# Kernel tuning notes

Measured on AMD Instinct MI355X. Metric: run time of the kernel, lower is better.

The kernel has to match this reference:

```python
import jax, jax.numpy as jnp
import numpy as np

B, T, D_IN, D_OUT = 4, 2048, 1024, 1024


def setup_inputs() -> dict:
    key = jax.random.key(0)
    k1, k2, k3, k4 = jax.random.split(key, 4)
    s = 0.02  # keep activations in a sane range
    x = jax.random.normal(k1, (B, T, D_IN), dtype=jnp.float32)
    Wq = jax.random.normal(k2, (D_IN, D_OUT), dtype=jnp.float32) * s
    Wk = jax.random.normal(k3, (D_IN, D_OUT), dtype=jnp.float32) * s
    Wv = jax.random.normal(k4, (D_IN, D_OUT), dtype=jnp.float32) * s
    return {"x": x, "Wq": Wq, "Wk": Wk, "Wv": Wv}


def reference(x, Wq, Wk, Wv):
    # Linear projections (torch Linear: y = x @ W^T, here W stored as [d_in, d_out])
    q = jnp.einsum('btd,de->bte', x, Wq)
    k = jnp.einsum('btd,de,->bte', x, Wk, jnp.float32(1.0)) if False else jnp.einsum('btd,de->bte', x, Wk)
    v = jnp.einsum('btd,de->bte', x, Wv)
    # Full [B, T, T] score matrix (faithful to the hand-rolled implementation)
    scores = jnp.einsum('bqe,bke->bqk', q, k)
    T_ = x.shape[1]
    causal = jnp.triu(jnp.ones((T_, T_), dtype=bool), k=1)  # True above diagonal
    scores = jnp.where(causal[None, :, :], -jnp.inf, scores)
    scale = 1.0 / jnp.sqrt(jnp.asarray(k.shape[-1], dtype=scores.dtype))
    attn = jax.nn.softmax(scores * scale, axis=-1)
    # dropout p=0.0 -> identity
    return jnp.einsum('bqk,bke->bqe', attn, v)
```

## Files before the change

kernel.cpp:

```cpp
#include <hip/hip_runtime.h>
#include <hip/hip_bf16.h>
#include <cstdint>

typedef __attribute__((ext_vector_type(8))) short short8;
typedef __attribute__((ext_vector_type(4))) short short4v;
typedef __attribute__((ext_vector_type(4))) float floatx4;
typedef unsigned short ushort;

__device__ __forceinline__ float bf2f(ushort u) {
  unsigned int x = ((unsigned int)u) << 16;
  return __builtin_bit_cast(float, x);
}
__device__ __forceinline__ ushort f2bf(float f) {
  unsigned int x = __builtin_bit_cast(unsigned int, f);
  x += 0x7fffu + ((x >> 16) & 1u);
  return (ushort)(x >> 16);
}

__device__ __forceinline__ void gload_lds16(const void* g, void* l) {
  __builtin_amdgcn_global_load_lds(
      (const __attribute__((address_space(1))) void*)g,
      (__attribute__((address_space(3))) void*)l, 16, 0, 0);
}


__global__ __launch_bounds__(256) void prep_kernel(const float* __restrict__ x,
                                                   const float* __restrict__ Wq,
                                                   const float* __restrict__ Wk,
                                                   const float* __restrict__ Wv,
                                                   ushort* __restrict__ xb,
                                                   ushort* __restrict__ Wt) {
  int bid = blockIdx.x;
  int tid = threadIdx.x;
  if (bid < 4096) {
    int i = bid * 256 + tid;
    const float4* xf = (const float4*)x;
    float4 a = xf[i * 2], b = xf[i * 2 + 1];
    short8 o;
    o[0] = (short)f2bf(a.x); o[1] = (short)f2bf(a.y);
    o[2] = (short)f2bf(a.z); o[3] = (short)f2bf(a.w);
    o[4] = (short)f2bf(b.x); o[5] = (short)f2bf(b.y);
    o[6] = (short)f2bf(b.z); o[7] = (short)f2bf(b.w);
    ((short8*)xb)[i] = o;
  } else {
    int t = bid - 4096;
    int z = t >> 8;
    int rem = t & 255;
    int c0 = (rem & 15) * 64;
    int r0 = (rem >> 4) * 64;
    const float* W = z == 0 ? Wq : (z == 1 ? Wk : Wv);
    ushort* O = Wt + (size_t)z * 1024 * 1024;
    __shared__ float tile[64][65];
#pragma unroll
    for (int i = 0; i < 4; ++i) {
      int c = tid + i * 256; int rr = c >> 4, q = c & 15;
      float4 v = *(const float4*)&W[(size_t)(r0 + rr) * 1024 + c0 + q * 4];
      tile[rr][q * 4 + 0] = v.x; tile[rr][q * 4 + 1] = v.y;
      tile[rr][q * 4 + 2] = v.z; tile[rr][q * 4 + 3] = v.w;
    }
    __syncthreads();
#pragma unroll
    for (int i = 0; i < 2; ++i) {
      int c = tid + i * 256; int oc = c >> 3, q = c & 7;
      short8 o;
#pragma unroll
      for (int j = 0; j < 8; ++j) o[j] = (short)f2bf(tile[q * 8 + j][oc]);
      *(short8*)&O[(size_t)(c0 + oc) * 1024 + r0 + q * 8] = o;
    }
  }
}


__global__ __launch_bounds__(512, 2) void qkv8_kernel(const ushort* __restrict__ A,
                                                      const ushort* __restrict__ Bm,
                                                      ushort* __restrict__ Qo,
                                                      ushort* __restrict__ Ko,
                                                      ushort* __restrict__ Vt) {
  __shared__ __align__(16) ushort lds[2][2][2][8192];

  const int tid = threadIdx.x;
  const int lane = tid & 63;
  const int wave = tid >> 6;
  const int wm = wave >> 2;
  const int wn = wave & 3;
  const int r15 = lane & 15;
  const int kg = lane >> 4;

  const int nwgx = 32, nwgy = 12;
  int orig = blockIdx.y * nwgx + blockIdx.x;
  int swz = (orig & 7) * ((nwgx * nwgy) >> 3) + (orig >> 3);
  int by = swz % nwgy;
  int bx = swz / nwgy;
  const int m0 = bx * 256;
  const int n0 = by * 256;

  const ushort* Ag = A + (size_t)m0 * 1024;
  const ushort* Bg = Bm + (size_t)n0 * 1024;

  const int NKT = 16;

  floatx4 acc[8][4] = {};

  auto stage = [&](int sidx) {
    int kt = sidx >> 2, hh = sidx & 3;
    int mat = hh & 1, kh = hh >> 1;
    ushort* dst = &lds[kt & 1][mat][kh][0];
    const ushort* src = mat ? Bg : Ag;
    int kbase = kt * 64 + kh * 32;
#pragma unroll
    for (int i = 0; i < 2; ++i) {
      int t = tid + i * 512;
      int d = t * 16;
      int L = d ^ (((d >> 7) & 3) << 4);
      int row = L >> 6;
      int colE = (L & 63) >> 1;
      gload_lds16(src + (size_t)row * 1024 + kbase + colE, dst + t * 8);
    }
  };

  auto ldA = [&](int buf, int ks, int m) -> short8 {
    int row = wm * 128 + m * 16 + r15;
    int L = row * 64 + kg * 16;
    int P = L ^ (((row >> 1) & 3) << 4);
    return *(const short8*)((const char*)&lds[buf][0][ks][0] + P);
  };
  auto ldB = [&](int buf, int ks, int n) -> short8 {
    int row = wn * 64 + n * 16 + r15;
    int L = row * 64 + kg * 16;
    int P = L ^ (((row >> 1) & 3) << 4);
    return *(const short8*)((const char*)&lds[buf][1][ks][0] + P);
  };

  for (int s = 0; s < 6; ++s) stage(s);
  asm volatile("s_waitcnt vmcnt(8)" ::: "memory");
  __builtin_amdgcn_s_barrier();

  short8 bfrag[4];
  int sidx = 6;
  for (int kt = 0; kt < NKT; ++kt) {
    int cur = kt & 1;
#pragma unroll
    for (int q = 0; q < 4; ++q) {
      const int ks = q >> 1;
      const int msub = (q & 1) * 4;
      short8 afrag[4];
      if ((q & 1) == 0) {
#pragma unroll
        for (int n = 0; n < 4; ++n) bfrag[n] = ldB(cur, ks, n);
      }
#pragma unroll
      for (int m = 0; m < 4; ++m) afrag[m] = ldA(cur, ks, msub + m);
      if (sidx < NKT * 4) stage(sidx);
      ++sidx;
      if (q & 1) asm volatile("s_waitcnt vmcnt(4)" ::: "memory");
      __builtin_amdgcn_s_barrier();
      __builtin_amdgcn_s_setprio(1);
#pragma unroll
      for (int m = 0; m < 4; ++m)
#pragma unroll
        for (int n = 0; n < 4; ++n)
          acc[msub + m][n] =
              __builtin_amdgcn_mfma_f32_16x16x32_bf16(afrag[m], bfrag[n], acc[msub + m][n], 0, 0, 0);
      __builtin_amdgcn_s_setprio(0);
      __builtin_amdgcn_s_barrier();
    }
  }

  const int z = n0 >> 10;
  const int rq = kg * 4;
  if (z < 2) {
    ushort* Cz = z == 0 ? Qo : Ko;
    const int cb = n0 & 1023;
#pragma unroll
    for (int m = 0; m < 8; ++m) {
#pragma unroll
      for (int n = 0; n < 4; ++n) {
        int gc = cb + wn * 64 + n * 16 + r15;
#pragma unroll
        for (int r = 0; r < 4; ++r) {
          int gr = m0 + wm * 128 + m * 16 + rq + r;
          Cz[(size_t)gr * 1024 + gc] = f2bf(acc[m][n][r]);
        }
      }
    }
  } else {
#pragma unroll
    for (int m = 0; m < 8; ++m) {
      int gr = m0 + wm * 128 + m * 16 + rq;
      int b = gr >> 11;
      int t = gr & 2047;
      ushort* Vb = Vt + (size_t)b * 1024 * 2048;
#pragma unroll
      for (int n = 0; n < 4; ++n) {
        int e = (n0 - 2048) + wn * 64 + n * 16 + r15;
        short4v o;
#pragma unroll
        for (int r = 0; r < 4; ++r) o[r] = (short)f2bf(acc[m][n][r]);
        *(short4v*)&Vb[(size_t)e * 2048 + t] = o;
      }
    }
  }
}


__global__ __launch_bounds__(256) void s_kernel(const ushort* __restrict__ Q,
                                                const ushort* __restrict__ K,
                                                ushort* __restrict__ S,
                                                float* __restrict__ Lpart) {
  int t = blockIdx.x;
  int qb = (int)((sqrtf(8.f * (float)t + 1.f) - 1.f) * 0.5f);
  while ((qb + 1) * (qb + 2) / 2 <= t) ++qb;
  while (qb * (qb + 1) / 2 > t) --qb;
  int kb = t - qb * (qb + 1) / 2;
  const size_t bi = blockIdx.y;
  const ushort* Ag = Q + bi * 2048 * 1024 + (size_t)qb * 128 * 1024;
  const ushort* Bg = K + bi * 2048 * 1024 + (size_t)kb * 128 * 1024;
  ushort* C = S + bi * 2048 * 2048;
  const int m0 = qb * 128, n0 = kb * 128;

  __shared__ __align__(16) ushort Asm[2][128 * 32];
  __shared__ __align__(16) ushort Bsm[2][128 * 32];
  __shared__ float rsum_lds[4][64];
  const int tid = threadIdx.x;
  const int lane = tid & 63;
  const int wave = tid >> 6;
  const int wrow = (wave >> 1) * 64;
  const int wcol = (wave & 1) * 64;
  const int r15 = lane & 15;
  const int kg = (lane >> 4) * 8;

  floatx4 acc[4][4] = {};

  auto stage = [&](int buf, int kt) {
    int k0 = kt * 32;
#pragma unroll
    for (int i = 0; i < 2; ++i) {
      int c = tid + i * 256;
      gload_lds16(Ag + (size_t)(c >> 2) * 1024 + k0 + (c & 3) * 8, &Asm[buf][c * 8]);
    }
#pragma unroll
    for (int i = 0; i < 2; ++i) {
      int c = tid + i * 256;
      gload_lds16(Bg + (size_t)(c >> 2) * 1024 + k0 + (c & 3) * 8, &Bsm[buf][c * 8]);
    }
  };

  stage(0, 0);
  for (int kt = 0; kt < 32; ++kt) {
    int cur = kt & 1;
    __syncthreads();
    if (kt + 1 < 32) stage(cur ^ 1, kt + 1);
    short8 af[4], bfr[4];
#pragma unroll
    for (int m = 0; m < 4; ++m)
      af[m] = *(const short8*)&Asm[cur][(wrow + m * 16 + r15) * 32 + kg];
#pragma unroll
    for (int n = 0; n < 4; ++n)
      bfr[n] = *(const short8*)&Bsm[cur][(wcol + n * 16 + r15) * 32 + kg];
#pragma unroll
    for (int m = 0; m < 4; ++m)
#pragma unroll
      for (int n = 0; n < 4; ++n)
        acc[m][n] = __builtin_amdgcn_mfma_f32_16x16x32_bf16(af[m], bfr[n], acc[m][n], 0, 0, 0);
  }

  const int rq = (lane >> 4) * 4;
  const float K2 = 0.03125f * 1.44269504f;
#pragma unroll
  for (int m = 0; m < 4; ++m) {
    float rs[4] = {0.f, 0.f, 0.f, 0.f};
#pragma unroll
    for (int n = 0; n < 4; ++n) {
      int gc = n0 + wcol + n * 16 + r15;
#pragma unroll
      for (int r = 0; r < 4; ++r) {
        int gr = m0 + wrow + m * 16 + rq + r;
        float ev = (gc <= gr) ? __builtin_amdgcn_exp2f(acc[m][n][r] * K2) : 0.f;
        C[(size_t)gr * 2048 + gc] = f2bf(ev);
        rs[r] += ev;
      }
    }
#pragma unroll
    for (int r = 0; r < 4; ++r) {
#pragma unroll
      for (int off = 1; off < 16; off <<= 1) rs[r] += __shfl_xor(rs[r], off, 64);
    }
    if (r15 == 0) {
#pragma unroll
      for (int r = 0; r < 4; ++r) rsum_lds[wave][m * 16 + rq + r] = rs[r];
    }
  }
  __syncthreads();
  if (tid < 128) {
    int h = tid >> 6;
    int lr = tid & 63;
    float v = rsum_lds[h * 2][lr] + rsum_lds[h * 2 + 1][lr];
    Lpart[((size_t)bi * 16 + kb) * 2048 + m0 + h * 64 + lr] = v;
  }
}


__global__ __launch_bounds__(256) void pv_kernel(const ushort* __restrict__ E,
                                                 const ushort* __restrict__ Vt,
                                                 const float* __restrict__ Lpart,
                                                 float* __restrict__ O) {
  const int qb = 15 - blockIdx.x;
  const int nb = blockIdx.y;
  const size_t bi = blockIdx.z;
  const int kTiles = (qb + 1) * 4;
  const ushort* Ag = E + bi * 2048 * 2048 + (size_t)qb * 128 * 2048;
  const ushort* Bg = Vt + bi * 1024 * 2048 + (size_t)nb * 128 * 2048;
  float* Ob = O + bi * 2048 * 1024;
  const int m0 = qb * 128, n0 = nb * 128;

  __shared__ __align__(16) ushort Asm[2][128 * 32];
  __shared__ __align__(16) ushort Bsm[2][128 * 32];
  __shared__ float ilp[128];
  const int tid = threadIdx.x;
  const int lane = tid & 63;
  const int wave = tid >> 6;
  const int wrow = (wave >> 1) * 64;
  const int wcol = (wave & 1) * 64;
  const int r15 = lane & 15;
  const int kg = (lane >> 4) * 8;

  floatx4 acc[4][4] = {};

  if (tid < 128) {
    float ssum = 0.f;
    for (int kb = 0; kb <= qb; ++kb)
      ssum += Lpart[((size_t)bi * 16 + kb) * 2048 + m0 + tid];
    ilp[tid] = 1.f / ssum;
  }

  auto stage = [&](int buf, int kt) {
    int k0 = kt * 32;
#pragma unroll
    for (int i = 0; i < 2; ++i) {
      int c = tid + i * 256;
      gload_lds16(Ag + (size_t)(c >> 2) * 2048 + k0 + (c & 3) * 8, &Asm[buf][c * 8]);
    }
#pragma unroll
    for (int i = 0; i < 2; ++i) {
      int c = tid + i * 256;
      gload_lds16(Bg + (size_t)(c >> 2) * 2048 + k0 + (c & 3) * 8, &Bsm[buf][c * 8]);
    }
  };

  stage(0, 0);
  for (int kt = 0; kt < kTiles; ++kt) {
    int cur = kt & 1;
    __syncthreads();
    if (kt + 1 < kTiles) stage(cur ^ 1, kt + 1);
    short8 af[4], bfr[4];
#pragma unroll
    for (int m = 0; m < 4; ++m)
      af[m] = *(const short8*)&Asm[cur][(wrow + m * 16 + r15) * 32 + kg];
#pragma unroll
    for (int n = 0; n < 4; ++n)
      bfr[n] = *(const short8*)&Bsm[cur][(wcol + n * 16 + r15) * 32 + kg];
#pragma unroll
    for (int m = 0; m < 4; ++m)
#pragma unroll
      for (int n = 0; n < 4; ++n)
        acc[m][n] = __builtin_amdgcn_mfma_f32_16x16x32_bf16(af[m], bfr[n], acc[m][n], 0, 0, 0);
  }

  const int rq = (lane >> 4) * 4;
#pragma unroll
  for (int m = 0; m < 4; ++m) {
#pragma unroll
    for (int r = 0; r < 4; ++r) {
      int lr = wrow + m * 16 + rq + r;
      float il = ilp[lr];
      int gr = m0 + lr;
#pragma unroll
      for (int n = 0; n < 4; ++n) {
        int gc = n0 + wcol + n * 16 + r15;
        Ob[(size_t)gr * 1024 + gc] = acc[m][n][r] * il;
      }
    }
  }
}


extern "C" void kernel_launch(void* const* d_in, const int* in_sizes, int n_in,
                              void* d_out, int out_size, void* d_ws, size_t ws_size,
                              hipStream_t stream) {
  const float* x  = (const float*)d_in[0];
  const float* Wq = (const float*)d_in[1];
  const float* Wk = (const float*)d_in[2];
  const float* Wv = (const float*)d_in[3];
  float* out = (float*)d_out;

  ushort* Xb  = (ushort*)d_ws;
  ushort* Wt  = Xb + (size_t)8192 * 1024;
  ushort* QK  = Wt + (size_t)3 * 1024 * 1024;
  ushort* Vt  = QK + (size_t)2 * 8192 * 1024;
  ushort* S   = Vt + (size_t)4 * 1024 * 2048;
  float*  Lpart = (float*)(S + (size_t)4 * 2048 * 2048);

  ushort* Qp = QK;
  ushort* Kp = QK + (size_t)8192 * 1024;

  hipLaunchKernelGGL(prep_kernel, dim3(4864), dim3(256), 0, stream, x, Wq, Wk, Wv, Xb, Wt);
  hipLaunchKernelGGL(qkv8_kernel, dim3(32, 12), dim3(512), 0, stream, Xb, Wt, Qp, Kp, Vt);
  hipLaunchKernelGGL(s_kernel, dim3(136, 4), dim3(256), 0, stream, Qp, Kp, S, Lpart);
  hipLaunchKernelGGL(pv_kernel, dim3(16, 8, 4), dim3(256), 0, stream, S, Vt, Lpart, out);
}
```

Measured before the change: 174.5 us.

## Balance causal PV workload by pairing short and long query tiles per block

The PV kernel now uses 64-row query half-tiles. Each block processes two of them, one from query block p and one from query block 15-p, so every block does about the same number of causal K tiles. This removes the load imbalance of the triangular schedule, where blocks with late query blocks ran much longer than early ones. The cost is smaller M tiles (less reuse of the B tile per MFMA step) and a changed grid, which must now be launched with x=16 (8 pairs × 2 halves). Launch code not shown.

```diff
diff --git a/kernel.cpp b/kernel.cpp
--- a/kernel.cpp
+++ b/kernel.cpp
@@ -300,44 +300,43 @@
 }
 
 
-__global__ __launch_bounds__(256) void pv_kernel(const ushort* __restrict__ E,
-                                                 const ushort* __restrict__ Vt,
-                                                 const float* __restrict__ Lpart,
-                                                 float* __restrict__ O) {
-  const int qb = 15 - blockIdx.x;
-  const int nb = blockIdx.y;
-  const size_t bi = blockIdx.z;
+__device__ __forceinline__ void pv_half(const ushort* __restrict__ E,
+                                        const ushort* __restrict__ Vt,
+                                        const float* __restrict__ Lpart,
+                                        float* __restrict__ O,
+                                        int bi, int qb, int mh, int nb,
+                                        ushort (*Asm)[64 * 32],
+                                        ushort (*Bsm)[128 * 32],
+                                        float* ilp) {
   const int kTiles = (qb + 1) * 4;
-  const ushort* Ag = E + bi * 2048 * 2048 + (size_t)qb * 128 * 2048;
-  const ushort* Bg = Vt + bi * 1024 * 2048 + (size_t)nb * 128 * 2048;
-  float* Ob = O + bi * 2048 * 1024;
-  const int m0 = qb * 128, n0 = nb * 128;
-
-  __shared__ __align__(16) ushort Asm[2][128 * 32];
-  __shared__ __align__(16) ushort Bsm[2][128 * 32];
-  __shared__ float ilp[128];
+  const int m0 = qb * 128 + mh * 64, n0 = nb * 128;
+  const ushort* Ag = E + (size_t)bi * 2048 * 2048 + (size_t)m0 * 2048;
+  const ushort* Bg = Vt + (size_t)bi * 1024 * 2048 + (size_t)n0 * 2048;
+  float* Ob = O + (size_t)bi * 2048 * 1024;
+
   const int tid = threadIdx.x;
   const int lane = tid & 63;
   const int wave = tid >> 6;
-  const int wrow = (wave >> 1) * 64;
+  const int wrow = (wave >> 1) * 32;
   const int wcol = (wave & 1) * 64;
   const int r15 = lane & 15;
   const int kg = (lane >> 4) * 8;
 
-  floatx4 acc[4][4] = {};
-
-  if (tid < 128) {
+  __syncthreads();
+
+  if (tid < 64) {
     float ssum = 0.f;
     for (int kb = 0; kb <= qb; ++kb)
       ssum += Lpart[((size_t)bi * 16 + kb) * 2048 + m0 + tid];
     ilp[tid] = 1.f / ssum;
   }
 
+  floatx4 acc[2][4] = {};
+
   auto stage = [&](int buf, int kt) {
     int k0 = kt * 32;
-#pragma unroll
-    for (int i = 0; i < 2; ++i) {
-      int c = tid + i * 256;
+    {
+      int c = tid;
       gload_lds16(Ag + (size_t)(c >> 2) * 2048 + k0 + (c & 3) * 8, &Asm[buf][c * 8]);
     }
 #pragma unroll
@@ -352,15 +351,15 @@
     int cur = kt & 1;
     __syncthreads();
     if (kt + 1 < kTiles) stage(cur ^ 1, kt + 1);
-    short8 af[4], bfr[4];
-#pragma unroll
-    for (int m = 0; m < 4; ++m)
+    short8 af[2], bfr[4];
+#pragma unroll
+    for (int m = 0; m < 2; ++m)
       af[m] = *(const short8*)&Asm[cur][(wrow + m * 16 + r15) * 32 + kg];
 #pragma unroll
     for (int n = 0; n < 4; ++n)
       bfr[n] = *(const short8*)&Bsm[cur][(wcol + n * 16 + r15) * 32 + kg];
 #pragma unroll
-    for (int m = 0; m < 4; ++m)
+    for (int m = 0; m < 2; ++m)
 #pragma unroll
       for (int n = 0; n < 4; ++n)
         acc[m][n] = __builtin_amdgcn_mfma_f32_16x16x32_bf16(af[m], bfr[n], acc[m][n], 0, 0, 0);
@@ -368,7 +367,7 @@
 
   const int rq = (lane >> 4) * 4;
 #pragma unroll
-  for (int m = 0; m < 4; ++m) {
+  for (int m = 0; m < 2; ++m) {
 #pragma unroll
     for (int r = 0; r < 4; ++r) {
       int lr = wrow + m * 16 + rq + r;
@@ -381,6 +380,24 @@
       }
     }
   }
+}
+
+__global__ __launch_bounds__(256) void pv_kernel(const ushort* __restrict__ E,
+                                                 const ushort* __restrict__ Vt,
+                                                 const float* __restrict__ Lpart,
+                                                 float* __restrict__ O) {
+  __shared__ __align__(16) ushort Asm[2][64 * 32];
+  __shared__ __align__(16) ushort Bsm[2][128 * 32];
+  __shared__ float ilp[64];
+
+  const int px = blockIdx.x;
+  const int p  = px >> 1;
+  const int mh = px & 1;
+  const int nb = blockIdx.y;
+  const int bi = blockIdx.z;
+
+  pv_half(E, Vt, Lpart, O, bi, p,      mh, nb, Asm, Bsm, ilp);
+  pv_half(E, Vt, Lpart, O, bi, 15 - p, mh, nb, Asm, Bsm, ilp);
 }
 
 
```

After: 176.2 us. Within noise of the previous version (+1.0%).
